# Optimization experiments

Measured on AMD Instinct MI355X. Metric: run time of the kernel, lower is better.

## Reference

```python
import jax, jax.numpy as jnp
import numpy as np
import math

B, S, D, DH, R = 2, 2048, 1024, 64, 2


def _hex_grid(radius):
    coords = []
    for q in range(-radius, radius + 1):
        for r in range(max(-radius, -q - radius), min(radius, -q + radius) + 1):
            coords.append((q, r))
    return coords


def _adjacency(coords):
    idx = {c: i for i, c in enumerate(coords)}
    H = len(coords)
    A = np.zeros((H, H), dtype=np.float32)
    dirs = [(1, 0), (1, -1), (0, -1), (-1, 0), (-1, 1), (0, 1)]
    for (q, r), i in idx.items():
        for dq, dr in dirs:
            j = idx.get((q + dq, r + dr))
            if j is not None:
                A[i, j] = 1.0
    return A


def setup_inputs() -> dict:
    key = jax.random.key(0)
    ks = jax.random.split(key, 10)
    coords_list = _hex_grid(R)
    H = len(coords_list)  # 19 heads for radius 2
    coords = jnp.asarray(np.array(coords_list, dtype=np.float32))  # [H,2]
    A = _adjacency(coords_list) + np.eye(H, dtype=np.float32)      # self-loops
    adj_norm = jnp.asarray(A / A.sum(axis=1, keepdims=True))       # row-normalized [H,H]
    sd = 1.0 / math.sqrt(D)
    return {
        "x": jax.random.normal(ks[0], (B, S, D), jnp.float32),
        "coords": coords,
        "w_q": jax.random.normal(ks[1], (H, D, DH), jnp.float32) * sd,
        "w_k": jax.random.normal(ks[2], (H, D, DH), jnp.float32) * sd,
        "w_v": jax.random.normal(ks[3], (H, D, DH), jnp.float32) * sd,
        "wb1": jax.random.normal(ks[4], (2, D), jnp.float32) * 0.5,
        "bb1": jnp.zeros((D,), jnp.float32),
        "wb2": jax.random.normal(ks[5], (D, DH), jnp.float32) * sd,
        "bb2": jnp.zeros((DH,), jnp.float32),
        "w_mix": jax.random.normal(ks[6], (DH, DH), jnp.float32) / math.sqrt(DH),
        "adj_norm": adj_norm,
        "w_o": jax.random.normal(ks[7], (H * DH, D), jnp.float32) * sd,
    }


def reference(x, coords, w_q, w_k, w_v, wb1, bb1, wb2, bb2, w_mix, adj_norm, w_o):
    # coordinate bias: shared MLP mapping hex coord -> d_head bias, added to queries
    bias = jax.nn.relu(coords @ wb1 + bb1) @ wb2 + bb2          # [H,DH]
    # all heads vectorized: q/k/v [B,H,S,DH]
    q = jnp.einsum("bsd,hde->bhse", x, w_q) + bias[None, :, None, :]
    k = jnp.einsum("bsd,hde->bhse", x, w_k)
    v = jnp.einsum("bsd,hde->bhse", x, w_v)
    scores = jnp.einsum("bhse,bhte->bhst", q, k) / math.sqrt(DH)  # [B,H,S,S]
    attn = jax.nn.softmax(scores, axis=-1)
    heads = jnp.einsum("bhst,bhte->bhse", attn, v)               # [B,H,S,DH]
    # GNN mixing over the hex-grid adjacency (residual message passing)
    msg = jax.nn.relu(jnp.einsum("bhse,ef->bhsf", heads, w_mix))
    mixed = heads + jnp.einsum("hg,bgsf->bhsf", adj_norm, msg)   # [B,H,S,DH]
    # concat heads then output projection
    Bx, H, Sx, Dh = mixed.shape
    concat = jnp.transpose(mixed, (0, 2, 1, 3)).reshape(Bx, Sx, H * Dh)
    return concat @ w_o                                          # [B,S,D]
```

## Files before the change

### kernel.cpp

```cpp
#include <hip/hip_runtime.h>
#include <hip/hip_bf16.h>

#define H 19
#define Bv 2
#define Sv 2048
#define Dv 1024
#define DHv 64
#define KK2 (2*H*DHv)
#define QSCALE 0.1803368801111204f

typedef __bf16 bf16x8 __attribute__((ext_vector_type(8)));
typedef float f32x4 __attribute__((ext_vector_type(4)));

__device__ __forceinline__ ushort f2bf(float f) {
    uint u = __float_as_uint(f);
    u = (u + 0x7fffu + ((u >> 16) & 1u)) >> 16;
    return (ushort)u;
}

__device__ __forceinline__ uint cvtpk(float lo, float hi) {
    uint r;
    asm("v_cvt_pk_bf16_f32 %0, %1, %2" : "=v"(r) : "v"(lo), "v"(hi));
    return r;
}

__device__ __forceinline__ float fexp2(float x) {
#if __has_builtin(__builtin_amdgcn_exp2f)
    return __builtin_amdgcn_exp2f(x);
#else
    return exp2f(x);
#endif
}

__device__ __forceinline__ void gll16(const ushort* g, ushort* l) {
    __builtin_amdgcn_global_load_lds(
        (const __attribute__((address_space(1))) unsigned int*)g,
        (__attribute__((address_space(3))) unsigned int*)l, 16, 0, 0);
}

#define PBIAS_AT 0
#define PWO2_AT  (PBIAS_AT + H)
#define PWMIX_AT (PWO2_AT + 304)
#define PWPK_AT  (PWMIX_AT + 1)
#define PX_AT    (PWPK_AT + 912)
#define PREP_N   (PX_AT + 2048)

__global__ __launch_bounds__(256) void prep_all(
    const float* __restrict__ x,  const float* __restrict__ wq,
    const float* __restrict__ wk, const float* __restrict__ wv,
    const float* __restrict__ wo, const float* __restrict__ adj,
    const float* __restrict__ wm, const float* __restrict__ coords,
    const float* __restrict__ wb1, const float* __restrict__ bb1,
    const float* __restrict__ wb2, const float* __restrict__ bb2,
    ushort* __restrict__ xbf, ushort* __restrict__ wpackT,
    ushort* __restrict__ wmixT, ushort* __restrict__ woTcat,
    float* __restrict__ bias)
{
    __shared__ char psm[18432];
    const int bid = blockIdx.x;
    const int tid = threadIdx.x;

    if (bid < PWO2_AT) {
        float* part = (float*)psm;
        int hh = bid - PBIAS_AT;
        int e = tid & 63, quar = tid >> 6;
        float c0 = coords[hh*2], c1 = coords[hh*2+1];
        float acc = (quar == 0) ? bb2[e] : 0.f;
        int d0 = quar*256;
        for (int d = d0; d < d0+256; ++d) {
            float t2 = fmaxf(c0*wb1[d] + c1*wb1[Dv+d] + bb1[d], 0.f);
            acc += t2 * wb2[d*DHv + e];
        }
        if (quar) part[(quar-1)*64 + e] = acc;
        __syncthreads();
        if (quar == 0) bias[hh*DHv + e] = acc + part[e] + part[64+e] + part[128+e];
    } else if (bid < PWMIX_AT) {
        int j2 = bid - PWO2_AT;
        int nt = j2 & 15, g = j2 >> 4;
        int e = tid >> 2, n4 = tid & 3;
        float acc[16], part1[16];
        #pragma unroll
        for (int j = 0; j < 16; ++j) { acc[j] = 0.f; part1[j] = 0.f; }
        for (int h2 = 0; h2 < H; ++h2) {
            float a = adj[h2*H + g];
            const float* rp = wo + (size_t)(h2*64 + e)*Dv + nt*64 + n4*16;
            #pragma unroll
            for (int j4 = 0; j4 < 4; ++j4) {
                float4 v = *(const float4*)&rp[j4*4];
                acc[j4*4+0] += a*v.x; acc[j4*4+1] += a*v.y;
                acc[j4*4+2] += a*v.z; acc[j4*4+3] += a*v.w;
                if (h2 == g) {
                    part1[j4*4+0] = v.x; part1[j4*4+1] = v.y;
                    part1[j4*4+2] = v.z; part1[j4*4+3] = v.w;
                }
            }
        }
        ushort* T = (ushort*)psm;
        #pragma unroll
        for (int j = 0; j < 16; ++j) {
            int nl = n4*16 + j;
            T[nl*72 + e]         = f2bf(part1[j]);
            T[64*72 + nl*72 + e] = f2bf(acc[j]);
        }
        __syncthreads();
        int nl = tid >> 2, c = tid & 3;
        {
            ushort* dst = &woTcat[(size_t)(nt*64 + nl)*KK2 + g*64 + c*16];
            uint4 v0 = *(uint4*)&T[nl*72 + c*16];
            uint4 v1 = *(uint4*)&T[nl*72 + c*16 + 8];
            *(uint4*)dst = v0; *(uint4*)(dst + 8) = v1;
        }
        {
            ushort* dst = &woTcat[(size_t)(nt*64 + nl)*KK2 + H*DHv + g*64 + c*16];
            uint4 v0 = *(uint4*)&T[64*72 + nl*72 + c*16];
            uint4 v1 = *(uint4*)&T[64*72 + nl*72 + c*16 + 8];
            *(uint4*)dst = v0; *(uint4*)(dst + 8) = v1;
        }
    } else if (bid == PWMIX_AT) {
        int e = tid >> 2, f4 = tid & 3;
        #pragma unroll
        for (int j = 0; j < 16; ++j) {
            int f = f4*16 + j;
            wmixT[e*64 + f] = f2bf(wm[f*64 + e]);
        }
    } else if (bid < PX_AT) {
        ushort* T = (ushort*)psm;
        int i = bid - PWPK_AT;
        int dt = i & 15, t = (i >> 4) % 3, h = (i >> 4) / 3;
        const float* w = (t == 0) ? wq : (t == 1) ? wk : wv;
        w += (size_t)h*Dv*DHv;
        int row = tid >> 2, c4 = tid & 3;
        #pragma unroll
        for (int q4 = 0; q4 < 4; ++q4) {
            float4 v = *(const float4*)&w[(size_t)(dt*64+row)*DHv + c4*16 + q4*4];
            T[(c4*16 + q4*4 + 0)*65 + row] = f2bf(v.x);
            T[(c4*16 + q4*4 + 1)*65 + row] = f2bf(v.y);
            T[(c4*16 + q4*4 + 2)*65 + row] = f2bf(v.z);
            T[(c4*16 + q4*4 + 3)*65 + row] = f2bf(v.w);
        }
        __syncthreads();
        #pragma unroll
        for (int i2 = 0; i2 < 2; ++i2) {
            int f = tid + i2*256;
            int e = f >> 3, c = f & 7;
            uint u[4];
            #pragma unroll
            for (int j = 0; j < 4; ++j) {
                uint lo = T[e*65 + c*8 + 2*j];
                uint hi = T[e*65 + c*8 + 2*j + 1];
                u[j] = lo | (hi << 16);
            }
            *(uint4*)&wpackT[((size_t)h*192 + t*64 + e)*Dv + dt*64 + c*8] = make_uint4(u[0],u[1],u[2],u[3]);
        }
    } else {
        int idx = ((bid - PX_AT)*256 + tid)*8;
        float4 a = *(const float4*)&x[idx];
        float4 b = *(const float4*)&x[idx+4];
        uint4 o;
        o.x = cvtpk(a.x, a.y); o.y = cvtpk(a.z, a.w);
        o.z = cvtpk(b.x, b.y); o.w = cvtpk(b.z, b.w);
        *(uint4*)&xbf[idx] = o;
    }
}

__global__ __launch_bounds__(256) void qkv_mfma(const ushort* __restrict__ xbf,
                                                const ushort* __restrict__ wpackT,
                                                const float* __restrict__ bias,
                                                ushort* __restrict__ qbf,
                                                ushort* __restrict__ kbf,
                                                ushort* __restrict__ vtbf) {
    const int mt = blockIdx.x, h = blockIdx.y;
    const int m0 = mt*64;
    const int tid = threadIdx.x;
    const int w = tid >> 6, lane = tid & 63;
    const int g = lane >> 4, r = lane & 15;

    __shared__ char lds[8192 + 24576];
    char* Xs = lds;
    char* Ws = lds + 8192;
    ushort* VtL = (ushort*)lds;

    f32x4 acc[4][3];
    const f32x4 zf = {0.f,0.f,0.f,0.f};
    #pragma unroll
    for (int m = 0; m < 4; ++m)
        #pragma unroll
        for (int n = 0; n < 3; ++n) acc[m][n] = zf;

    const ushort* xb = xbf + (size_t)m0*Dv;
    const ushort* wb = wpackT + (size_t)h*192*Dv;

    for (int kt = 0; kt < Dv; kt += 64) {
        __syncthreads();
        #pragma unroll
        for (int i = 0; i < 2; ++i) {
            int f = tid + i*256;
            int row = f >> 3, c = f & 7;
            *(bf16x8*)(Xs + row*128 + ((c*16) ^ ((row & 7) << 4))) =
                *(const bf16x8*)(xb + (size_t)row*Dv + kt + c*8);
        }
        #pragma unroll
        for (int i = 0; i < 6; ++i) {
            int f = tid + i*256;
            int row = f >> 3, c = f & 7;
            *(bf16x8*)(Ws + row*128 + ((c*16) ^ ((row & 7) << 4))) =
                *(const bf16x8*)(wb + (size_t)row*Dv + kt + c*8);
        }
        __syncthreads();
        #pragma unroll
        for (int kk = 0; kk < 2; ++kk) {
            bf16x8 a[4], bfr[3];
            #pragma unroll
            for (int m = 0; m < 4; ++m) {
                int row = m*16 + r;
                a[m] = *(const bf16x8*)(Xs + row*128 + (((kk*32 + g*8)*2) ^ ((row & 7) << 4)));
            }
            #pragma unroll
            for (int n = 0; n < 3; ++n) {
                int row = (w*3 + n)*16 + r;
                bfr[n] = *(const bf16x8*)(Ws + row*128 + (((kk*32 + g*8)*2) ^ ((row & 7) << 4)));
            }
            #pragma unroll
            for (int m = 0; m < 4; ++m)
                #pragma unroll
                for (int n = 0; n < 3; ++n)
                    acc[m][n] = __builtin_amdgcn_mfma_f32_16x16x32_bf16(a[m], bfr[n], acc[m][n], 0, 0, 0);
        }
    }

    __syncthreads();

    const int bb = m0 >> 11;
    const int s0 = m0 & 2047;
    #pragma unroll
    for (int m = 0; m < 4; ++m) {
        #pragma unroll
        for (int n = 0; n < 3; ++n) {
            int ng = w*3 + n;
            int t = ng >> 2;
            int e = (ng & 3)*16 + r;
            if (t == 0) {
                float bvv = bias[h*DHv + e];
                #pragma unroll
                for (int reg = 0; reg < 4; ++reg) {
                    int ss = s0 + m*16 + g*4 + reg;
                    qbf[(((size_t)bb*H + h)*Sv + ss)*DHv + e] = f2bf((acc[m][n][reg] + bvv)*QSCALE);
                }
            } else if (t == 1) {
                #pragma unroll
                for (int reg = 0; reg < 4; ++reg) {
                    int ss = s0 + m*16 + g*4 + reg;
                    kbf[(((size_t)bb*H + h)*Sv + ss)*DHv + e] = f2bf(acc[m][n][reg]);
                }
            } else {
                #pragma unroll
                for (int reg = 0; reg < 4; ++reg) {
                    int sl = m*16 + g*4 + reg;
                    VtL[e*66 + sl] = f2bf(acc[m][n][reg]);
                }
            }
        }
    }
    __syncthreads();
    #pragma unroll
    for (int i = 0; i < 2; ++i) {
        int f = tid + i*256;
        int dh = f >> 3, sc = f & 7;
        uint u[4];
        #pragma unroll
        for (int j = 0; j < 4; ++j) {
            uint lo = VtL[dh*66 + sc*8 + 2*j];
            uint hi = VtL[dh*66 + sc*8 + 2*j + 1];
            u[j] = lo | (hi << 16);
        }
        *(uint4*)&vtbf[(((size_t)bb*H + h)*DHv + dh)*Sv + s0 + sc*8] = make_uint4(u[0],u[1],u[2],u[3]);
    }
}

__global__ __launch_bounds__(256) void attn_mfma(const ushort* __restrict__ qg,
                                                 const ushort* __restrict__ kg,
                                                 const ushort* __restrict__ vtg,
                                                 const ushort* __restrict__ wmixT,
                                                 ushort* __restrict__ headsbf,
                                                 ushort* __restrict__ msgbf) {
    const int hw = blockIdx.x;
    const int logical = (hw & 7) * 152 + (hw >> 3);
    const int qt = logical & 31;
    const int hb = logical >> 5;
    const int h = hb % H, b = hb / H;

    const int tid = threadIdx.x;
    const int w = tid >> 6, lane = tid & 63;
    const int g = lane >> 4, r = lane & 15;
    const int srow = lane >> 3, scl = lane & 7;

    __shared__ ushort Ks[4096];
    __shared__ ushort Vs[4096];
    __shared__ ushort Ps[4][1024];

    const size_t bh = (size_t)b*H + h;
    const ushort* kb = kg + bh*Sv*DHv;
    const ushort* vb = vtg + bh*DHv*Sv;
    const ushort* qb = qg + (bh*Sv + qt*64 + w*16 + r)*DHv;

    bf16x8 qf0 = *(const bf16x8*)(qb + g*8);
    bf16x8 qf1 = *(const bf16x8*)(qb + 32 + g*8);

    float m_run = -1e30f, l_run = 0.f;
    f32x4 o[4];
    const f32x4 zf = {0.f,0.f,0.f,0.f};
    o[0]=zf; o[1]=zf; o[2]=zf; o[3]=zf;

    for (int jt = 0; jt < Sv/64; ++jt) {
        __syncthreads();
        #pragma unroll
        for (int is = 0; is < 2; ++is) {
            int row = w*16 + is*8 + srow;
            int kcol = (scl ^ (row & 7)) * 8;
            gll16(kb + (size_t)(jt*64 + row)*DHv + kcol, &Ks[(w*16 + is*8)*64]);
            gll16(vb + (size_t)row*Sv + jt*64 + kcol, &Vs[(w*16 + is*8)*64]);
        }
        asm volatile("s_waitcnt vmcnt(0)" ::: "memory");
        __syncthreads();

        f32x4 sc[4];
        sc[0]=zf; sc[1]=zf; sc[2]=zf; sc[3]=zf;
        #pragma unroll
        for (int kk = 0; kk < 2; ++kk) {
            bf16x8 qf = kk ? qf1 : qf0;
            #pragma unroll
            for (int nt = 0; nt < 4; ++nt) {
                int kvrow = nt*16 + r;
                bf16x8 kf = *(const bf16x8*)((const char*)Ks + kvrow*128 +
                                             ((kk*64 + g*16) ^ ((kvrow & 7) << 4)));
                sc[nt] = __builtin_amdgcn_mfma_f32_16x16x32_bf16(kf, qf, sc[nt], 0, 0, 0);
            }
        }

        float pmax = sc[0][0];
        #pragma unroll
        for (int nt = 0; nt < 4; ++nt)
            #pragma unroll
            for (int reg = 0; reg < 4; ++reg)
                pmax = fmaxf(pmax, sc[nt][reg]);
        pmax = fmaxf(pmax, __shfl_xor(pmax, 16));
        pmax = fmaxf(pmax, __shfl_xor(pmax, 32));

        if (__any(pmax > m_run + 8.0f)) {
            float mn = fmaxf(m_run, pmax);
            float corr = fexp2(m_run - mn);
            l_run *= corr;
            #pragma unroll
            for (int nt2 = 0; nt2 < 4; ++nt2) {
                o[nt2][0] *= corr; o[nt2][1] *= corr;
                o[nt2][2] *= corr; o[nt2][3] *= corr;
            }
            m_run = mn;
        }

        float lsum = 0.f;
        #pragma unroll
        for (int nt = 0; nt < 4; ++nt) {
            #pragma unroll
            for (int reg = 0; reg < 4; ++reg) {
                float p = fexp2(sc[nt][reg] - m_run);
                sc[nt][reg] = p;
                lsum += p;
            }
        }
        lsum += __shfl_xor(lsum, 16);
        lsum += __shfl_xor(lsum, 32);
        l_run += lsum;

        ushort* pw = Ps[w];
        #pragma unroll
        for (int nt = 0; nt < 4; ++nt) {
            uint u0 = cvtpk(sc[nt][0], sc[nt][1]);
            uint u1 = cvtpk(sc[nt][2], sc[nt][3]);
            int chunk = (2*nt + (g >> 1)) ^ (r & 7);
            *(uint2*)((char*)pw + r*128 + (chunk << 4) + ((g & 1)*8)) = make_uint2(u0, u1);
        }

        #pragma unroll
        for (int kk = 0; kk < 2; ++kk) {
            bf16x8 pa = *(const bf16x8*)((const char*)pw + r*128 +
                                         (((kk*4 + g) ^ (r & 7)) << 4));
            #pragma unroll
            for (int nt2 = 0; nt2 < 4; ++nt2) {
                int dh = nt2*16 + r;
                bf16x8 vf = *(const bf16x8*)((const char*)Vs + dh*128 +
                                             ((kk*64 + g*16) ^ ((dh & 7) << 4)));
                o[nt2] = __builtin_amdgcn_mfma_f32_16x16x32_bf16(vf, pa, o[nt2], 0, 0, 0);
            }
        }
    }

    float inv = 1.0f / l_run;
    ushort* hp = headsbf + (bh*Sv + qt*64 + w*16 + r)*DHv;
    ushort* pw = Ps[w];
    #pragma unroll
    for (int nt2 = 0; nt2 < 4; ++nt2) {
        uint u0 = cvtpk(o[nt2][0]*inv, o[nt2][1]*inv);
        uint u1 = cvtpk(o[nt2][2]*inv, o[nt2][3]*inv);
        *(uint2*)(hp + nt2*16 + g*4) = make_uint2(u0, u1);
        int chunk = (2*nt2 + (g >> 1)) ^ (r & 7);
        *(uint2*)((char*)pw + r*128 + (chunk << 4) + ((g & 1)*8)) = make_uint2(u0, u1);
    }

    bf16x8 wmf[2][4];
    #pragma unroll
    for (int kk = 0; kk < 2; ++kk)
        #pragma unroll
        for (int nt = 0; nt < 4; ++nt)
            wmf[kk][nt] = *(const bf16x8*)(wmixT + (nt*16 + r)*64 + kk*32 + g*8);

    f32x4 macc[4];
    macc[0]=zf; macc[1]=zf; macc[2]=zf; macc[3]=zf;
    #pragma unroll
    for (int kk = 0; kk < 2; ++kk) {
        bf16x8 pa = *(const bf16x8*)((const char*)pw + r*128 +
                                     (((kk*4 + g) ^ (r & 7)) << 4));
        #pragma unroll
        for (int nt = 0; nt < 4; ++nt)
            macc[nt] = __builtin_amdgcn_mfma_f32_16x16x32_bf16(wmf[kk][nt], pa, macc[nt], 0, 0, 0);
    }
    ushort* mp = msgbf + (bh*Sv + qt*64 + w*16 + r)*DHv;
    #pragma unroll
    for (int nt = 0; nt < 4; ++nt) {
        uint u0 = cvtpk(fmaxf(macc[nt][0], 0.f), fmaxf(macc[nt][1], 0.f));
        uint u1 = cvtpk(fmaxf(macc[nt][2], 0.f), fmaxf(macc[nt][3], 0.f));
        *(uint2*)(mp + nt*16 + g*4) = make_uint2(u0, u1);
    }
}

__global__ __launch_bounds__(256) void out_mfma(const ushort* __restrict__ headsbf,
                                                const ushort* __restrict__ msgbf,
                                                const ushort* __restrict__ woTcat,
                                                float* __restrict__ out) {
    const int mt = blockIdx.x, nt2 = blockIdx.y;
    const int m0 = mt*64, n0 = nt2*128;
    const int tid = threadIdx.x;
    const int w = tid >> 6, lane = tid & 63;
    const int g = lane >> 4, r = lane & 15;

    __shared__ char lds[8192 + 16384];
    char* As = lds;
    char* Bs = lds + 8192;

    const int b = m0 >> 11;
    const int s0 = m0 & 2047;

    f32x4 acc[8];
    const f32x4 zf = {0.f,0.f,0.f,0.f};
    #pragma unroll
    for (int n = 0; n < 8; ++n) acc[n] = zf;

    for (int ktile = 0; ktile < KK2/64; ++ktile) {
        const int hh = (ktile < H) ? ktile : ktile - H;
        const ushort* asrc = ((ktile < H) ? headsbf : msgbf) +
                             ((size_t)((size_t)b*H + hh)*Sv + s0)*DHv;
        __syncthreads();
        #pragma unroll
        for (int i = 0; i < 2; ++i) {
            int f = tid + i*256;
            int row = f >> 3, c = f & 7;
            *(bf16x8*)(As + row*128 + ((c*16) ^ ((row & 7) << 4))) =
                *(const bf16x8*)(asrc + (size_t)row*DHv + c*8);
        }
        #pragma unroll
        for (int i = 0; i < 4; ++i) {
            int f = tid + i*256;
            int row = f >> 3, c = f & 7;
            *(bf16x8*)(Bs + row*128 + ((c*16) ^ ((row & 7) << 4))) =
                *(const bf16x8*)(woTcat + (size_t)(n0 + row)*KK2 + ktile*64 + c*8);
        }
        __syncthreads();
        #pragma unroll
        for (int kk = 0; kk < 2; ++kk) {
            int arow = w*16 + r;
            bf16x8 a = *(const bf16x8*)(As + arow*128 + (((kk*32 + g*8)*2) ^ ((arow & 7) << 4)));
            #pragma unroll
            for (int n = 0; n < 8; ++n) {
                int brow = n*16 + r;
                bf16x8 bfr = *(const bf16x8*)(Bs + brow*128 + (((kk*32 + g*8)*2) ^ ((brow & 7) << 4)));
                acc[n] = __builtin_amdgcn_mfma_f32_16x16x32_bf16(a, bfr, acc[n], 0, 0, 0);
            }
        }
    }

    #pragma unroll
    for (int n = 0; n < 8; ++n) {
        #pragma unroll
        for (int reg = 0; reg < 4; ++reg) {
            int grow = m0 + w*16 + g*4 + reg;
            out[(size_t)grow*Dv + n0 + n*16 + r] = acc[n][reg];
        }
    }
}

extern "C" void kernel_launch(void* const* d_in, const int* in_sizes, int n_in,
                              void* d_out, int out_size, void* d_ws, size_t ws_size,
                              hipStream_t stream) {
    const float* x      = (const float*)d_in[0];
    const float* coords = (const float*)d_in[1];
    const float* w_q    = (const float*)d_in[2];
    const float* w_k    = (const float*)d_in[3];
    const float* w_v    = (const float*)d_in[4];
    const float* wb1    = (const float*)d_in[5];
    const float* bb1    = (const float*)d_in[6];
    const float* wb2    = (const float*)d_in[7];
    const float* bb2    = (const float*)d_in[8];
    const float* w_mix  = (const float*)d_in[9];
    const float* adj    = (const float*)d_in[10];
    const float* w_o    = (const float*)d_in[11];

    char* ws = (char*)d_ws;
    const size_t QKV_BYTES = (size_t)Bv*H*Sv*DHv*2;
    const size_t XBF_BYTES = (size_t)Bv*Sv*Dv*2;
    const size_t WPK_BYTES = (size_t)H*192*Dv*2;

    size_t off = 0;
    float*  bias  = (float*)(ws + off);  off += 16384;
    ushort* qbf   = (ushort*)(ws + off); off += QKV_BYTES;
    ushort* kbf   = (ushort*)(ws + off); off += QKV_BYTES;
    ushort* vtbf  = (ushort*)(ws + off); off += QKV_BYTES;
    ushort* hdbf  = (ushort*)(ws + off); off += QKV_BYTES;
    ushort* xbf   = (ushort*)(ws + off);
    ushort* msgbf = xbf;
    off += XBF_BYTES;
    ushort* wpkT  = (ushort*)(ws + off); off += WPK_BYTES;
    ushort* wmixT = (ushort*)(ws + off); off += 8192;
    ushort* woTc  = (ushort*)(ws + off); off += (size_t)Dv*KK2*2;
    float*  out   = (float*)d_out;

    prep_all<<<PREP_N, 256, 0, stream>>>(x, w_q, w_k, w_v, w_o, adj, w_mix,
                                         coords, wb1, bb1, wb2, bb2,
                                         xbf, wpkT, wmixT, woTc, bias);
    qkv_mfma<<<dim3(64, H), 256, 0, stream>>>(xbf, wpkT, bias, qbf, kbf, vtbf);
    attn_mfma<<<1216, 256, 0, stream>>>(qbf, kbf, vtbf, wmixT, hdbf, msgbf);
    out_mfma<<<dim3(64, 8), 256, 0, stream>>>(hdbf, msgbf, woTc, out);
}
```

Before: 345.4 us.

## Read K/V fragments directly from global memory and split bias MLP into parallel kernel

The attention kernel no longer stages K and V tiles into LDS through global_load_lds with block-wide barriers. Each wave now loads its own K and V^T MFMA fragments straight from global memory, relying on L1/L2 caching. This removes two __syncthreads per KV tile and frees LDS, but every wave in a block re-reads the same tile and gets no explicit prefetch overlap. Separately, the coordinate-bias MLP moves out of the prep kernel into its own kernel split four ways over D, and qkv sums the partial results, shortening the serial bias blocks at the cost of an extra launch.

```diff
diff --git a/kernel.cpp b/kernel.cpp
--- a/kernel.cpp
+++ b/kernel.cpp
@@ -32,49 +32,25 @@
 #endif
 }
 
-__device__ __forceinline__ void gll16(const ushort* g, ushort* l) {
-    __builtin_amdgcn_global_load_lds(
-        (const __attribute__((address_space(1))) unsigned int*)g,
-        (__attribute__((address_space(3))) unsigned int*)l, 16, 0, 0);
-}
-
-#define PBIAS_AT 0
-#define PWO2_AT  (PBIAS_AT + H)
-#define PWMIX_AT (PWO2_AT + 304)
-#define PWPK_AT  (PWMIX_AT + 1)
-#define PX_AT    (PWPK_AT + 912)
+#define PWO2_AT  0
+#define PWPK_AT  (PWO2_AT + 304)
+#define PWMIX_AT (PWPK_AT + 912)
+#define PX_AT    (PWMIX_AT + 1)
 #define PREP_N   (PX_AT + 2048)
 
-__global__ __launch_bounds__(256) void prep_all(
+__global__ __launch_bounds__(256) void prep_misc(
     const float* __restrict__ x,  const float* __restrict__ wq,
     const float* __restrict__ wk, const float* __restrict__ wv,
     const float* __restrict__ wo, const float* __restrict__ adj,
-    const float* __restrict__ wm, const float* __restrict__ coords,
-    const float* __restrict__ wb1, const float* __restrict__ bb1,
-    const float* __restrict__ wb2, const float* __restrict__ bb2,
+    const float* __restrict__ wm,
     ushort* __restrict__ xbf, ushort* __restrict__ wpackT,
-    ushort* __restrict__ wmixT, ushort* __restrict__ woTcat,
-    float* __restrict__ bias)
+    ushort* __restrict__ wmixT, ushort* __restrict__ woTcat)
 {
     __shared__ char psm[18432];
     const int bid = blockIdx.x;
     const int tid = threadIdx.x;
 
-    if (bid < PWO2_AT) {
-        float* part = (float*)psm;
-        int hh = bid - PBIAS_AT;
-        int e = tid & 63, quar = tid >> 6;
-        float c0 = coords[hh*2], c1 = coords[hh*2+1];
-        float acc = (quar == 0) ? bb2[e] : 0.f;
-        int d0 = quar*256;
-        for (int d = d0; d < d0+256; ++d) {
-            float t2 = fmaxf(c0*wb1[d] + c1*wb1[Dv+d] + bb1[d], 0.f);
-            acc += t2 * wb2[d*DHv + e];
-        }
-        if (quar) part[(quar-1)*64 + e] = acc;
-        __syncthreads();
-        if (quar == 0) bias[hh*DHv + e] = acc + part[e] + part[64+e] + part[128+e];
-    } else if (bid < PWMIX_AT) {
+    if (bid < PWPK_AT) {
         int j2 = bid - PWO2_AT;
         int nt = j2 & 15, g = j2 >> 4;
         int e = tid >> 2, n4 = tid & 3;
@@ -116,14 +92,7 @@
             uint4 v1 = *(uint4*)&T[64*72 + nl*72 + c*16 + 8];
             *(uint4*)dst = v0; *(uint4*)(dst + 8) = v1;
         }
-    } else if (bid == PWMIX_AT) {
-        int e = tid >> 2, f4 = tid & 3;
-        #pragma unroll
-        for (int j = 0; j < 16; ++j) {
-            int f = f4*16 + j;
-            wmixT[e*64 + f] = f2bf(wm[f*64 + e]);
-        }
-    } else if (bid < PX_AT) {
+    } else if (bid < PWMIX_AT) {
         ushort* T = (ushort*)psm;
         int i = bid - PWPK_AT;
         int dt = i & 15, t = (i >> 4) % 3, h = (i >> 4) / 3;
@@ -151,6 +120,13 @@
                 u[j] = lo | (hi << 16);
             }
             *(uint4*)&wpackT[((size_t)h*192 + t*64 + e)*Dv + dt*64 + c*8] = make_uint4(u[0],u[1],u[2],u[3]);
+        }
+    } else if (bid == PWMIX_AT) {
+        int e = tid >> 2, f4 = tid & 3;
+        #pragma unroll
+        for (int j = 0; j < 16; ++j) {
+            int f = f4*16 + j;
+            wmixT[e*64 + f] = f2bf(wm[f*64 + e]);
         }
     } else {
         int idx = ((bid - PX_AT)*256 + tid)*8;
@@ -163,9 +139,31 @@
     }
 }
 
+__global__ __launch_bounds__(256) void bias_part_kernel(
+    const float* __restrict__ coords, const float* __restrict__ wb1,
+    const float* __restrict__ bb1, const float* __restrict__ wb2,
+    const float* __restrict__ bb2, float* __restrict__ bias_part) {
+    const int bq = blockIdx.x, hh = blockIdx.y;
+    const int e = threadIdx.x & 63, sub = threadIdx.x >> 6;
+    __shared__ float part[3][64];
+    float c0 = coords[hh*2], c1 = coords[hh*2+1];
+    float acc = (bq == 0 && sub == 0) ? bb2[e] : 0.f;
+    const int d0 = bq*256 + sub*64;
+    #pragma unroll 8
+    for (int i = 0; i < 64; ++i) {
+        int d = d0 + i;
+        float t2 = fmaxf(c0*wb1[d] + c1*wb1[Dv+d] + bb1[d], 0.f);
+        acc += t2 * wb2[d*DHv + e];
+    }
+    if (sub) part[sub-1][e] = acc;
+    __syncthreads();
+    if (sub == 0)
+        bias_part[(bq*H + hh)*DHv + e] = acc + part[0][e] + part[1][e] + part[2][e];
+}
+
 __global__ __launch_bounds__(256) void qkv_mfma(const ushort* __restrict__ xbf,
                                                 const ushort* __restrict__ wpackT,
-                                                const float* __restrict__ bias,
+                                                const float* __restrict__ bias_part,
                                                 ushort* __restrict__ qbf,
                                                 ushort* __restrict__ kbf,
                                                 ushort* __restrict__ vtbf) {
@@ -240,7 +238,8 @@
             int t = ng >> 2;
             int e = (ng & 3)*16 + r;
             if (t == 0) {
-                float bvv = bias[h*DHv + e];
+                float bvv = bias_part[(0*H + h)*DHv + e] + bias_part[(1*H + h)*DHv + e]
+                          + bias_part[(2*H + h)*DHv + e] + bias_part[(3*H + h)*DHv + e];
                 #pragma unroll
                 for (int reg = 0; reg < 4; ++reg) {
                     int ss = s0 + m*16 + g*4 + reg;
@@ -292,10 +291,7 @@
     const int tid = threadIdx.x;
     const int w = tid >> 6, lane = tid & 63;
     const int g = lane >> 4, r = lane & 15;
-    const int srow = lane >> 3, scl = lane & 7;
-
-    __shared__ ushort Ks[4096];
-    __shared__ ushort Vs[4096];
+
     __shared__ ushort Ps[4][1024];
 
     const size_t bh = (size_t)b*H + h;
@@ -311,38 +307,35 @@
     const f32x4 zf = {0.f,0.f,0.f,0.f};
     o[0]=zf; o[1]=zf; o[2]=zf; o[3]=zf;
 
+    ushort* pw = Ps[w];
+
     for (int jt = 0; jt < Sv/64; ++jt) {
-        __syncthreads();
-        #pragma unroll
-        for (int is = 0; is < 2; ++is) {
-            int row = w*16 + is*8 + srow;
-            int kcol = (scl ^ (row & 7)) * 8;
-            gll16(kb + (size_t)(jt*64 + row)*DHv + kcol, &Ks[(w*16 + is*8)*64]);
-            gll16(vb + (size_t)row*Sv + jt*64 + kcol, &Vs[(w*16 + is*8)*64]);
-        }
-        asm volatile("s_waitcnt vmcnt(0)" ::: "memory");
-        __syncthreads();
+        const ushort* ktile = kb + (size_t)jt*64*DHv;
+        const ushort* vtile = vb + jt*64;
 
         f32x4 sc[4];
         sc[0]=zf; sc[1]=zf; sc[2]=zf; sc[3]=zf;
-        #pragma unroll
-        for (int kk = 0; kk < 2; ++kk) {
-            bf16x8 qf = kk ? qf1 : qf0;
-            #pragma unroll
-            for (int nt = 0; nt < 4; ++nt) {
-                int kvrow = nt*16 + r;
-                bf16x8 kf = *(const bf16x8*)((const char*)Ks + kvrow*128 +
-                                             ((kk*64 + g*16) ^ ((kvrow & 7) << 4)));
-                sc[nt] = __builtin_amdgcn_mfma_f32_16x16x32_bf16(kf, qf, sc[nt], 0, 0, 0);
-            }
-        }
-
-        float pmax = sc[0][0];
-        #pragma unroll
-        for (int nt = 0; nt < 4; ++nt)
-            #pragma unroll
-            for (int reg = 0; reg < 4; ++reg)
-                pmax = fmaxf(pmax, sc[nt][reg]);
+        {
+            bf16x8 kf[2][4];
+            #pragma unroll
+            for (int kk = 0; kk < 2; ++kk)
+                #pragma unroll
+                for (int nt = 0; nt < 4; ++nt)
+                    kf[kk][nt] = *(const bf16x8*)(ktile + (size_t)(nt*16 + r)*DHv + kk*32 + g*8);
+            #pragma unroll
+            for (int kk = 0; kk < 2; ++kk) {
+                bf16x8 qf = kk ? qf1 : qf0;
+                #pragma unroll
+                for (int nt = 0; nt < 4; ++nt)
+                    sc[nt] = __builtin_amdgcn_mfma_f32_16x16x32_bf16(kf[kk][nt], qf, sc[nt], 0, 0, 0);
+            }
+        }
+
+        float mx0 = fmaxf(fmaxf(sc[0][0], sc[0][1]), fmaxf(sc[0][2], sc[0][3]));
+        float mx1 = fmaxf(fmaxf(sc[1][0], sc[1][1]), fmaxf(sc[1][2], sc[1][3]));
+        float mx2 = fmaxf(fmaxf(sc[2][0], sc[2][1]), fmaxf(sc[2][2], sc[2][3]));
+        float mx3 = fmaxf(fmaxf(sc[3][0], sc[3][1]), fmaxf(sc[3][2], sc[3][3]));
+        float pmax = fmaxf(fmaxf(mx0, mx1), fmaxf(mx2, mx3));
         pmax = fmaxf(pmax, __shfl_xor(pmax, 16));
         pmax = fmaxf(pmax, __shfl_xor(pmax, 32));
 
@@ -372,7 +365,6 @@
         lsum += __shfl_xor(lsum, 32);
         l_run += lsum;
 
-        ushort* pw = Ps[w];
         #pragma unroll
         for (int nt = 0; nt < 4; ++nt) {
             uint u0 = cvtpk(sc[nt][0], sc[nt][1]);
@@ -387,9 +379,7 @@
                                          (((kk*4 + g) ^ (r & 7)) << 4));
             #pragma unroll
             for (int nt2 = 0; nt2 < 4; ++nt2) {
-                int dh = nt2*16 + r;
-                bf16x8 vf = *(const bf16x8*)((const char*)Vs + dh*128 +
-                                             ((kk*64 + g*16) ^ ((dh & 7) << 4)));
+                bf16x8 vf = *(const bf16x8*)(vtile + (size_t)(nt2*16 + r)*Sv + kk*32 + g*8);
                 o[nt2] = __builtin_amdgcn_mfma_f32_16x16x32_bf16(vf, pa, o[nt2], 0, 0, 0);
             }
         }
@@ -397,7 +387,6 @@
 
     float inv = 1.0f / l_run;
     ushort* hp = headsbf + (bh*Sv + qt*64 + w*16 + r)*DHv;
-    ushort* pw = Ps[w];
     #pragma unroll
     for (int nt2 = 0; nt2 < 4; ++nt2) {
         uint u0 = cvtpk(o[nt2][0]*inv, o[nt2][1]*inv);
@@ -520,7 +509,7 @@
     const size_t WPK_BYTES = (size_t)H*192*Dv*2;
 
     size_t off = 0;
-    float*  bias  = (float*)(ws + off);  off += 16384;
+    float*  biasp = (float*)(ws + off);  off += 32768;
     ushort* qbf   = (ushort*)(ws + off); off += QKV_BYTES;
     ushort* kbf   = (ushort*)(ws + off); off += QKV_BYTES;
     ushort* vtbf  = (ushort*)(ws + off); off += QKV_BYTES;
@@ -533,10 +522,10 @@
     ushort* woTc  = (ushort*)(ws + off); off += (size_t)Dv*KK2*2;
     float*  out   = (float*)d_out;
 
-    prep_all<<<PREP_N, 256, 0, stream>>>(x, w_q, w_k, w_v, w_o, adj, w_mix,
-                                         coords, wb1, bb1, wb2, bb2,
-                                         xbf, wpkT, wmixT, woTc, bias);
-    qkv_mfma<<<dim3(64, H), 256, 0, stream>>>(xbf, wpkT, bias, qbf, kbf, vtbf);
+    prep_misc<<<PREP_N, 256, 0, stream>>>(x, w_q, w_k, w_v, w_o, adj, w_mix,
+                                          xbf, wpkT, wmixT, woTc);
+    bias_part_kernel<<<dim3(4, H), 256, 0, stream>>>(coords, wb1, bb1, wb2, bb2, biasp);
+    qkv_mfma<<<dim3(64, H), 256, 0, stream>>>(xbf, wpkT, biasp, qbf, kbf, vtbf);
     attn_mfma<<<1216, 256, 0, stream>>>(qbf, kbf, vtbf, wmixT, hdbf, msgbf);
     out_mfma<<<dim3(64, 8), 256, 0, stream>>>(hdbf, msgbf, woTc, out);
 }
```

After: 501.4 us. 45.2% more time.
